# Optimization experiments

Measured on AMD Instinct MI355X. Metric: run time of the kernel, lower is better.

The kernel has to match this reference:

```python
import jax, jax.numpy as jnp
import numpy as np

D_MODEL = 1024
N_HEAD = 16
HEAD_SIZE = D_MODEL // N_HEAD


def setup_inputs() -> dict:
    key = jax.random.key(0)
    ks = jax.random.split(key, 7)
    B, T, E = 2, 2048, D_MODEL
    scale = 0.02
    return {
        "q": jax.random.normal(ks[0], (B, T, E), dtype=jnp.float32),
        "k": jax.random.normal(ks[1], (B, T, E), dtype=jnp.float32),
        "v": jax.random.normal(ks[2], (B, T, E), dtype=jnp.float32),
        "Wq": jax.random.normal(ks[3], (E, E), dtype=jnp.float32) * scale,
        "Wk": jax.random.normal(ks[4], (E, E), dtype=jnp.float32) * scale,
        "Wv": jax.random.normal(ks[5], (E, E), dtype=jnp.float32) * scale,
        "Wo": jax.random.normal(ks[6], (E, E), dtype=jnp.float32) * scale,
    }


def reference(q, k, v, Wq, Wk, Wv, Wo):
    B, T, E = q.shape
    # torch nn.Linear(bias=False): y = x @ W.T
    qh = (q @ Wq.T).reshape(B, T, N_HEAD, HEAD_SIZE).transpose(0, 2, 1, 3)  # [B,H,T,Dh]
    kh = (k @ Wk.T).reshape(B, T, N_HEAD, HEAD_SIZE).transpose(0, 2, 1, 3)
    vh = (v @ Wv.T).reshape(B, T, N_HEAD, HEAD_SIZE).transpose(0, 2, 1, 3)

    scale = 1.0 / jnp.sqrt(jnp.asarray(HEAD_SIZE, dtype=q.dtype))
    wei = jnp.einsum("bhqd,bhkd->bhqk", qh, kh) * scale  # [B,H,T,T]

    # causal mask (tril): positions j > i set to -inf
    causal = jnp.tril(jnp.ones((T, T), dtype=bool))
    wei = jnp.where(causal, wei, jnp.asarray(-jnp.inf, dtype=wei.dtype))

    attn = jax.nn.softmax(wei, axis=-1)
    out = jnp.einsum("bhqk,bhkd->bhqd", attn, vh)  # [B,H,T,Dh]
    out = out.transpose(0, 2, 1, 3).reshape(B, T, E)
    return out @ Wo.T  # dropout p=0.0 -> identity
```

## Files before the change

### kernel.cpp

```cpp
#include <hip/hip_runtime.h>
#include <hip/hip_bf16.h>
#include <cstddef>
#include <cstdint>

#define B_SZ   2
#define T_SEQ  2048
#define E_DIM  1024
#define N_HEAD 16
#define HEAD   64

typedef unsigned short u16;
typedef unsigned int u32;
using frag8 = __attribute__((ext_vector_type(8))) short;
using f32x4 = __attribute__((ext_vector_type(4))) float;

__device__ inline u16 f2bf(float x) {
    __hip_bfloat16 h = __float2bfloat16(x);
    return *reinterpret_cast<u16*>(&h);
}

__device__ inline void gl2lds16(const void* g, void* l) {
    auto gp = reinterpret_cast<const __attribute__((address_space(1))) unsigned int*>(
        reinterpret_cast<uintptr_t>(g));
    auto lp = reinterpret_cast<__attribute__((address_space(3))) unsigned int*>(
        reinterpret_cast<uintptr_t>(l));
    __builtin_amdgcn_global_load_lds(gp, lp, 16, 0, 0);
}

struct CastArgs {
    const float* src[7];
    u16* dst[7];
    int n[7];
    float scale[7];
};

__global__ __launch_bounds__(256) void cast_f32_bf16(CastArgs a) {
    const int t = blockIdx.y;
    const int i0 = (blockIdx.x * 256 + threadIdx.x) * 8;
    if (i0 >= a.n[t]) return;
    const float sc = a.scale[t];
    const float4 f0 = *(const float4*)(a.src[t] + i0);
    const float4 f1 = *(const float4*)(a.src[t] + i0 + 4);
    union { u16 s[8]; uint4 v; } r;
    r.s[0] = f2bf(f0.x * sc); r.s[1] = f2bf(f0.y * sc);
    r.s[2] = f2bf(f0.z * sc); r.s[3] = f2bf(f0.w * sc);
    r.s[4] = f2bf(f1.x * sc); r.s[5] = f2bf(f1.y * sc);
    r.s[6] = f2bf(f1.z * sc); r.s[7] = f2bf(f1.w * sc);
    *(uint4*)(a.dst[t] + i0) = r.v;
}

__device__ inline void gemm_core(const u16* __restrict__ X,
                                 const u16* __restrict__ W,
                                 void* __restrict__ Yv, int mode,
                                 int bm0, int bn0) {
    __shared__ u16 As[64 * 64];
    __shared__ u16 Bs[128 * 64];

    const int tid = threadIdx.x;
    const int w = tid >> 6;
    const int lane = tid & 63;
    const int ln = lane & 15;
    const int quad = lane >> 4;
    const int wm = (w & 1) * 32;
    const int wn = (w >> 1) * 64;

    const int l8 = lane >> 3;
    const int g = (lane & 7) ^ l8;

    const u16* Ag = X + (size_t)(bm0 + w * 16 + l8) * 1024 + g * 8;
    const u16* Bg = W + (size_t)(bn0 + w * 32 + l8) * 1024 + g * 8;
    const int al = __builtin_amdgcn_readfirstlane(w * 1024);
    const int bl = __builtin_amdgcn_readfirstlane(w * 2048);

    const f32x4 zf = {0.f, 0.f, 0.f, 0.f};
    f32x4 acc[2][4];
#pragma unroll
    for (int mi = 0; mi < 2; ++mi)
#pragma unroll
        for (int nj = 0; nj < 4; ++nj) acc[mi][nj] = zf;

    const int sw = ln & 7;

    for (int k0 = 0; k0 < 1024; k0 += 64) {
        gl2lds16(Ag + k0, As + al);
        gl2lds16(Ag + 8 * 1024 + k0, As + al + 512);
#pragma unroll
        for (int i = 0; i < 4; ++i)
            gl2lds16(Bg + i * 8 * 1024 + k0, Bs + bl + i * 512);
        __syncthreads();

        frag8 a[2][2], b[4][2];
#pragma unroll
        for (int kc = 0; kc < 2; ++kc) {
            const int slot = ((kc * 4 + quad) ^ sw) * 8;
#pragma unroll
            for (int mi = 0; mi < 2; ++mi)
                a[mi][kc] = *(const frag8*)(As + (wm + mi * 16 + ln) * 64 + slot);
#pragma unroll
            for (int nj = 0; nj < 4; ++nj)
                b[nj][kc] = *(const frag8*)(Bs + (wn + nj * 16 + ln) * 64 + slot);
        }
#pragma unroll
        for (int kc = 0; kc < 2; ++kc)
#pragma unroll
            for (int mi = 0; mi < 2; ++mi)
#pragma unroll
                for (int nj = 0; nj < 4; ++nj)
                    acc[mi][nj] = __builtin_amdgcn_mfma_f32_16x16x32_bf16(
                        a[mi][kc], b[nj][kc], acc[mi][nj], 0, 0, 0);
        __syncthreads();
    }

#pragma unroll
    for (int mi = 0; mi < 2; ++mi)
#pragma unroll
        for (int nj = 0; nj < 4; ++nj)
#pragma unroll
            for (int reg = 0; reg < 4; ++reg) {
                const int m = bm0 + wm + mi * 16 + quad * 4 + reg;
                const int n = bn0 + wn + nj * 16 + ln;
                if (mode == 1) {
                    ((float*)Yv)[(size_t)m * E_DIM + n] = acc[mi][nj][reg];
                } else {
                    const int b_ = m >> 11, t_ = m & (T_SEQ - 1);
                    const int h_ = n >> 6, d_ = n & (HEAD - 1);
                    const size_t idx = (mode == 0)
                        ? (((size_t)(b_ * N_HEAD + h_)) * T_SEQ + t_) * HEAD + d_
                        : (((size_t)(b_ * N_HEAD + h_)) * HEAD + d_) * T_SEQ + t_;
                    ((u16*)Yv)[idx] = f2bf(acc[mi][nj][reg]);
                }
            }
}

struct QkvArgs {
    const u16* X[3];
    const u16* W[3];
    u16* Y[3];
};

__global__ __launch_bounds__(256) void gemm_qkv(QkvArgs a) {
    const int z = blockIdx.z;
    gemm_core(a.X[z], a.W[z], a.Y[z], z == 2 ? 2 : 0,
              blockIdx.x * 64, blockIdx.y * 128);
}

__global__ __launch_bounds__(256) void gemm_out(const u16* __restrict__ X,
                                                const u16* __restrict__ W,
                                                float* __restrict__ Y) {
    gemm_core(X, W, Y, 1, blockIdx.x * 64, blockIdx.y * 128);
}

__global__ __launch_bounds__(256, 4) void attn_mfma(const u16* __restrict__ Qh,
                                                    const u16* __restrict__ Kh,
                                                    const u16* __restrict__ Vt_g,
                                                    u16* __restrict__ Aa) {
    __shared__ u16 Ks[2][64 * 64];
    __shared__ u16 Vs[2][64 * 64];

    const int tid = threadIdx.x;
    const int w = tid >> 6;
    const int lane = tid & 63;
    const int ln = lane & 15;
    const int quad = lane >> 4;

    const int i = blockIdx.x;
    const int half = i >> 8;
    const int r_ = i & 255;
    const int bh = r_ >> 3;
    const int j = r_ & 7;
    const int qt = half ? j : (15 - j);
    const int q0 = qt * 128;
    const int qw = q0 + w * 32;

    const size_t base = (size_t)bh * T_SEQ * HEAD;
    const u16* Qb = Qh + base;
    const u16* Kb = Kh + base;
    const u16* Vtb = Vt_g + base;

    const int l8 = lane >> 3;
    const int g = (lane & 7) ^ l8;
    const int kls = __builtin_amdgcn_readfirstlane(w * 16 * 64);
    const int vls = __builtin_amdgcn_readfirstlane(w * 16 * 64);

    frag8 qf[2][2];
#pragma unroll
    for (int qq = 0; qq < 2; ++qq)
#pragma unroll
        for (int kc = 0; kc < 2; ++kc)
            qf[qq][kc] = *(const frag8*)(Qb + (size_t)(qw + qq * 16 + ln) * HEAD +
                                         kc * 32 + quad * 8);

    const f32x4 zf = {0.f, 0.f, 0.f, 0.f};
    f32x4 o[4][2];
    float rsl[2] = {0.f, 0.f};
#pragma unroll
    for (int dt = 0; dt < 4; ++dt)
#pragma unroll
        for (int qq = 0; qq < 2; ++qq) o[dt][qq] = zf;

    const int ktiles = 2 * qt + 2;

    {
        const int k0 = 0;
#pragma unroll
        for (int it = 0; it < 2; ++it) {
            const int rb = w * 16 + it * 8;
            gl2lds16(Kb + (size_t)(k0 + rb + l8) * HEAD + g * 8,
                     &Ks[0][0] + kls + it * 512);
            gl2lds16(Vtb + (size_t)(rb + l8) * T_SEQ + k0 + g * 8,
                     &Vs[0][0] + vls + it * 512);
        }
    }

    const int sw = ln & 7;

    for (int kt = 0; kt < ktiles; ++kt) {
        const int k0 = kt * 64;
        const int buf = kt & 1;
        __syncthreads();

        if (kt + 1 < ktiles) {
            const int k1 = k0 + 64;
#pragma unroll
            for (int it = 0; it < 2; ++it) {
                const int rb = w * 16 + it * 8;
                gl2lds16(Kb + (size_t)(k1 + rb + l8) * HEAD + g * 8,
                         &Ks[buf ^ 1][0] + kls + it * 512);
                gl2lds16(Vtb + (size_t)(rb + l8) * T_SEQ + k1 + g * 8,
                         &Vs[buf ^ 1][0] + vls + it * 512);
            }
        }

        if (k0 <= qw + 31) {
            f32x4 st[4][2];
#pragma unroll
            for (int kk = 0; kk < 4; ++kk)
#pragma unroll
                for (int qq = 0; qq < 2; ++qq) st[kk][qq] = zf;
#pragma unroll
            for (int kc = 0; kc < 2; ++kc) {
                const int slot = ((kc * 4 + quad) ^ sw) * 8;
#pragma unroll
                for (int kk = 0; kk < 4; ++kk) {
                    const frag8 kf = *(const frag8*)(&Ks[buf][0] + (kk * 16 + ln) * 64 + slot);
#pragma unroll
                    for (int qq = 0; qq < 2; ++qq)
                        st[kk][qq] = __builtin_amdgcn_mfma_f32_16x16x32_bf16(
                            kf, qf[qq][kc], st[kk][qq], 0, 0, 0);
                }
            }

            const bool msk = (k0 + 63 > qw);
            u32 pk[4][2][2];
#pragma unroll
            for (int kk = 0; kk < 4; ++kk)
#pragma unroll
                for (int qq = 0; qq < 2; ++qq) {
                    float e[4];
#pragma unroll
                    for (int reg = 0; reg < 4; ++reg) {
                        const int key = k0 + kk * 16 + quad * 4 + reg;
                        const int qg = qw + qq * 16 + ln;
                        float ev = __expf(st[kk][qq][reg]);
                        if (msk) ev = (key <= qg) ? ev : 0.f;
                        e[reg] = ev;
                        rsl[qq] += ev;
                    }
                    pk[kk][qq][0] = ((u32)f2bf(e[1]) << 16) | f2bf(e[0]);
                    pk[kk][qq][1] = ((u32)f2bf(e[3]) << 16) | f2bf(e[2]);
                }

            const int hsel = quad >> 1;
            const int s_lo = ((quad & 1) * 2) * 16 + ln;
            const int s_hi = s_lo + 16;
#pragma unroll
            for (int kc = 0; kc < 2; ++kc) {
                union { frag8 f; u32 d[4]; } pb[2];
#pragma unroll
                for (int qq = 0; qq < 2; ++qq) {
                    const u32 a00 = __shfl(pk[kc * 2][qq][0], s_lo, 64);
                    const u32 a01 = __shfl(pk[kc * 2][qq][1], s_lo, 64);
                    const u32 a02 = __shfl(pk[kc * 2][qq][0], s_hi, 64);
                    const u32 a03 = __shfl(pk[kc * 2][qq][1], s_hi, 64);
                    const u32 a10 = __shfl(pk[kc * 2 + 1][qq][0], s_lo, 64);
                    const u32 a11 = __shfl(pk[kc * 2 + 1][qq][1], s_lo, 64);
                    const u32 a12 = __shfl(pk[kc * 2 + 1][qq][0], s_hi, 64);
                    const u32 a13 = __shfl(pk[kc * 2 + 1][qq][1], s_hi, 64);
                    pb[qq].d[0] = hsel ? a10 : a00;
                    pb[qq].d[1] = hsel ? a11 : a01;
                    pb[qq].d[2] = hsel ? a12 : a02;
                    pb[qq].d[3] = hsel ? a13 : a03;
                }
                const int slot = ((kc * 4 + quad) ^ sw) * 8;
#pragma unroll
                for (int dt = 0; dt < 4; ++dt) {
                    const frag8 vf = *(const frag8*)(&Vs[buf][0] + (dt * 16 + ln) * 64 + slot);
#pragma unroll
                    for (int qq = 0; qq < 2; ++qq)
                        o[dt][qq] = __builtin_amdgcn_mfma_f32_16x16x32_bf16(
                            vf, pb[qq].f, o[dt][qq], 0, 0, 0);
                }
            }
        }
    }

#pragma unroll
    for (int qq = 0; qq < 2; ++qq) {
        rsl[qq] += __shfl_xor(rsl[qq], 16, 64);
        rsl[qq] += __shfl_xor(rsl[qq], 32, 64);
    }
    const float inv0 = 1.f / rsl[0];
    const float inv1 = 1.f / rsl[1];
    const int b_ = bh >> 4, h_ = bh & (N_HEAD - 1);
#pragma unroll
    for (int qq = 0; qq < 2; ++qq) {
        const float inv = qq ? inv1 : inv0;
        const int qg = qw + qq * 16 + ln;
        u16* rowp = Aa + ((size_t)(b_ * T_SEQ + qg)) * E_DIM + h_ * HEAD;
#pragma unroll
        for (int dt = 0; dt < 4; ++dt)
#pragma unroll
            for (int rp = 0; rp < 2; ++rp) {
                const u32 v = ((u32)f2bf(o[dt][qq][2 * rp + 1] * inv) << 16) |
                              f2bf(o[dt][qq][2 * rp] * inv);
                *(u32*)(rowp + dt * 16 + quad * 4 + rp * 2) = v;
            }
    }
}

extern "C" void kernel_launch(void* const* d_in, const int* in_sizes, int n_in,
                              void* d_out, int out_size, void* d_ws, size_t ws_size,
                              hipStream_t stream) {
    const float* q  = (const float*)d_in[0];
    const float* k  = (const float*)d_in[1];
    const float* v  = (const float*)d_in[2];
    const float* Wq = (const float*)d_in[3];
    const float* Wk = (const float*)d_in[4];
    const float* Wv = (const float*)d_in[5];
    const float* Wo = (const float*)d_in[6];

    u16* ws = (u16*)d_ws;
    const size_t M4 = (size_t)4 * 1024 * 1024;
    const size_t M1 = (size_t)1024 * 1024;
    u16* qb  = ws;
    u16* kb  = ws + M4;
    u16* vb  = ws + 2 * M4;
    u16* Wqb = ws + 3 * M4;
    u16* Wkb = ws + 3 * M4 + M1;
    u16* Wvb = ws + 3 * M4 + 2 * M1;
    u16* Wob = ws + 3 * M4 + 3 * M1;
    u16* Qh  = ws + 4 * M4;
    u16* Kh  = ws + 5 * M4;
    u16* Vht = ws + 6 * M4;
    u16* Aa  = ws + 7 * M4;

    CastArgs ca;
    ca.src[0] = q;  ca.src[1] = k;  ca.src[2] = v;
    ca.src[3] = Wq; ca.src[4] = Wk; ca.src[5] = Wv; ca.src[6] = Wo;
    ca.dst[0] = qb;  ca.dst[1] = kb;  ca.dst[2] = vb;
    ca.dst[3] = Wqb; ca.dst[4] = Wkb; ca.dst[5] = Wvb; ca.dst[6] = Wob;
    ca.n[0] = ca.n[1] = ca.n[2] = (int)M4;
    ca.n[3] = ca.n[4] = ca.n[5] = ca.n[6] = (int)M1;
    ca.scale[0] = ca.scale[1] = ca.scale[2] = 1.f;
    ca.scale[3] = 0.125f;
    ca.scale[4] = ca.scale[5] = ca.scale[6] = 1.f;
    cast_f32_bf16<<<dim3(2048, 7), 256, 0, stream>>>(ca);

    QkvArgs ga;
    ga.X[0] = qb;  ga.X[1] = kb;  ga.X[2] = vb;
    ga.W[0] = Wqb; ga.W[1] = Wkb; ga.W[2] = Wvb;
    ga.Y[0] = Qh;  ga.Y[1] = Kh;  ga.Y[2] = Vht;
    gemm_qkv<<<dim3(64, 8, 3), 256, 0, stream>>>(ga);

    attn_mfma<<<dim3(512), 256, 0, stream>>>(Qh, Kh, Vht, Aa);

    gemm_out<<<dim3(64, 8), 256, 0, stream>>>(Aa, Wob, (float*)d_out);
}
```

Before: 220.3 us.

## Enlarge GEMM tiles to 128x128 and shrink attention query tiles to 64

```diff
diff --git a/kernel.cpp b/kernel.cpp
--- a/kernel.cpp
+++ b/kernel.cpp
@@ -53,7 +53,7 @@
                                  const u16* __restrict__ W,
                                  void* __restrict__ Yv, int mode,
                                  int bm0, int bn0) {
-    __shared__ u16 As[64 * 64];
+    __shared__ u16 As[128 * 64];
     __shared__ u16 Bs[128 * 64];
 
     const int tid = threadIdx.x;
@@ -61,49 +61,47 @@
     const int lane = tid & 63;
     const int ln = lane & 15;
     const int quad = lane >> 4;
-    const int wm = (w & 1) * 32;
+    const int wm = (w & 1) * 64;
     const int wn = (w >> 1) * 64;
 
     const int l8 = lane >> 3;
     const int g = (lane & 7) ^ l8;
 
-    const u16* Ag = X + (size_t)(bm0 + w * 16 + l8) * 1024 + g * 8;
+    const u16* Ag = X + (size_t)(bm0 + w * 32 + l8) * 1024 + g * 8;
     const u16* Bg = W + (size_t)(bn0 + w * 32 + l8) * 1024 + g * 8;
-    const int al = __builtin_amdgcn_readfirstlane(w * 1024);
-    const int bl = __builtin_amdgcn_readfirstlane(w * 2048);
+    const int sls = __builtin_amdgcn_readfirstlane(w * 32 * 64);
 
     const f32x4 zf = {0.f, 0.f, 0.f, 0.f};
-    f32x4 acc[2][4];
-#pragma unroll
-    for (int mi = 0; mi < 2; ++mi)
+    f32x4 acc[4][4];
+#pragma unroll
+    for (int mi = 0; mi < 4; ++mi)
 #pragma unroll
         for (int nj = 0; nj < 4; ++nj) acc[mi][nj] = zf;
 
     const int sw = ln & 7;
 
     for (int k0 = 0; k0 < 1024; k0 += 64) {
-        gl2lds16(Ag + k0, As + al);
-        gl2lds16(Ag + 8 * 1024 + k0, As + al + 512);
-#pragma unroll
-        for (int i = 0; i < 4; ++i)
-            gl2lds16(Bg + i * 8 * 1024 + k0, Bs + bl + i * 512);
+#pragma unroll
+        for (int it = 0; it < 4; ++it) {
+            gl2lds16(Ag + (size_t)it * 8 * 1024 + k0, As + sls + it * 512);
+            gl2lds16(Bg + (size_t)it * 8 * 1024 + k0, Bs + sls + it * 512);
+        }
         __syncthreads();
 
-        frag8 a[2][2], b[4][2];
+        frag8 a[4][2], b[4][2];
 #pragma unroll
         for (int kc = 0; kc < 2; ++kc) {
             const int slot = ((kc * 4 + quad) ^ sw) * 8;
 #pragma unroll
-            for (int mi = 0; mi < 2; ++mi)
-                a[mi][kc] = *(const frag8*)(As + (wm + mi * 16 + ln) * 64 + slot);
-#pragma unroll
-            for (int nj = 0; nj < 4; ++nj)
-                b[nj][kc] = *(const frag8*)(Bs + (wn + nj * 16 + ln) * 64 + slot);
+            for (int t = 0; t < 4; ++t) {
+                a[t][kc] = *(const frag8*)(As + (wm + t * 16 + ln) * 64 + slot);
+                b[t][kc] = *(const frag8*)(Bs + (wn + t * 16 + ln) * 64 + slot);
+            }
         }
 #pragma unroll
         for (int kc = 0; kc < 2; ++kc)
 #pragma unroll
-            for (int mi = 0; mi < 2; ++mi)
+            for (int mi = 0; mi < 4; ++mi)
 #pragma unroll
                 for (int nj = 0; nj < 4; ++nj)
                     acc[mi][nj] = __builtin_amdgcn_mfma_f32_16x16x32_bf16(
@@ -112,7 +110,7 @@
     }
 
 #pragma unroll
-    for (int mi = 0; mi < 2; ++mi)
+    for (int mi = 0; mi < 4; ++mi)
 #pragma unroll
         for (int nj = 0; nj < 4; ++nj)
 #pragma unroll
@@ -141,13 +139,13 @@
 __global__ __launch_bounds__(256) void gemm_qkv(QkvArgs a) {
     const int z = blockIdx.z;
     gemm_core(a.X[z], a.W[z], a.Y[z], z == 2 ? 2 : 0,
-              blockIdx.x * 64, blockIdx.y * 128);
+              blockIdx.x * 128, blockIdx.y * 128);
 }
 
 __global__ __launch_bounds__(256) void gemm_out(const u16* __restrict__ X,
                                                 const u16* __restrict__ W,
                                                 float* __restrict__ Y) {
-    gemm_core(X, W, Y, 1, blockIdx.x * 64, blockIdx.y * 128);
+    gemm_core(X, W, Y, 1, blockIdx.x * 128, blockIdx.y * 128);
 }
 
 __global__ __launch_bounds__(256, 4) void attn_mfma(const u16* __restrict__ Qh,
@@ -164,13 +162,13 @@
     const int quad = lane >> 4;
 
     const int i = blockIdx.x;
-    const int half = i >> 8;
-    const int r_ = i & 255;
-    const int bh = r_ >> 3;
-    const int j = r_ & 7;
-    const int qt = half ? j : (15 - j);
-    const int q0 = qt * 128;
-    const int qw = q0 + w * 32;
+    const int half = i >> 9;
+    const int r_ = i & 511;
+    const int bh = r_ >> 4;
+    const int j = r_ & 15;
+    const int qt = half ? j : (31 - j);
+    const int q0 = qt * 64;
+    const int qw = q0 + w * 16;
 
     const size_t base = (size_t)bh * T_SEQ * HEAD;
     const u16* Qb = Qh + base;
@@ -179,37 +177,26 @@
 
     const int l8 = lane >> 3;
     const int g = (lane & 7) ^ l8;
-    const int kls = __builtin_amdgcn_readfirstlane(w * 16 * 64);
-    const int vls = __builtin_amdgcn_readfirstlane(w * 16 * 64);
-
-    frag8 qf[2][2];
-#pragma unroll
-    for (int qq = 0; qq < 2; ++qq)
-#pragma unroll
-        for (int kc = 0; kc < 2; ++kc)
-            qf[qq][kc] = *(const frag8*)(Qb + (size_t)(qw + qq * 16 + ln) * HEAD +
-                                         kc * 32 + quad * 8);
+    const int sls = __builtin_amdgcn_readfirstlane(w * 16 * 64);
+
+    frag8 qf[2];
+#pragma unroll
+    for (int kc = 0; kc < 2; ++kc)
+        qf[kc] = *(const frag8*)(Qb + (size_t)(qw + ln) * HEAD + kc * 32 + quad * 8);
 
     const f32x4 zf = {0.f, 0.f, 0.f, 0.f};
-    f32x4 o[4][2];
-    float rsl[2] = {0.f, 0.f};
-#pragma unroll
-    for (int dt = 0; dt < 4; ++dt)
-#pragma unroll
-        for (int qq = 0; qq < 2; ++qq) o[dt][qq] = zf;
-
-    const int ktiles = 2 * qt + 2;
-
-    {
-        const int k0 = 0;
-#pragma unroll
-        for (int it = 0; it < 2; ++it) {
-            const int rb = w * 16 + it * 8;
-            gl2lds16(Kb + (size_t)(k0 + rb + l8) * HEAD + g * 8,
-                     &Ks[0][0] + kls + it * 512);
-            gl2lds16(Vtb + (size_t)(rb + l8) * T_SEQ + k0 + g * 8,
-                     &Vs[0][0] + vls + it * 512);
-        }
+    f32x4 o[4];
+    float rsl = 0.f;
+#pragma unroll
+    for (int dt = 0; dt < 4; ++dt) o[dt] = zf;
+
+    const int ktiles = qt + 1;
+
+#pragma unroll
+    for (int it = 0; it < 2; ++it) {
+        const int rb = w * 16 + it * 8;
+        gl2lds16(Kb + (size_t)(rb + l8) * HEAD + g * 8, &Ks[0][0] + sls + it * 512);
+        gl2lds16(Vtb + (size_t)(rb + l8) * T_SEQ + g * 8, &Vs[0][0] + sls + it * 512);
     }
 
     const int sw = ln & 7;
@@ -225,107 +212,86 @@
             for (int it = 0; it < 2; ++it) {
                 const int rb = w * 16 + it * 8;
                 gl2lds16(Kb + (size_t)(k1 + rb + l8) * HEAD + g * 8,
-                         &Ks[buf ^ 1][0] + kls + it * 512);
+                         &Ks[buf ^ 1][0] + sls + it * 512);
                 gl2lds16(Vtb + (size_t)(rb + l8) * T_SEQ + k1 + g * 8,
-                         &Vs[buf ^ 1][0] + vls + it * 512);
-            }
-        }
-
-        if (k0 <= qw + 31) {
-            f32x4 st[4][2];
-#pragma unroll
-            for (int kk = 0; kk < 4; ++kk)
-#pragma unroll
-                for (int qq = 0; qq < 2; ++qq) st[kk][qq] = zf;
-#pragma unroll
-            for (int kc = 0; kc < 2; ++kc) {
-                const int slot = ((kc * 4 + quad) ^ sw) * 8;
-#pragma unroll
-                for (int kk = 0; kk < 4; ++kk) {
-                    const frag8 kf = *(const frag8*)(&Ks[buf][0] + (kk * 16 + ln) * 64 + slot);
-#pragma unroll
-                    for (int qq = 0; qq < 2; ++qq)
-                        st[kk][qq] = __builtin_amdgcn_mfma_f32_16x16x32_bf16(
-                            kf, qf[qq][kc], st[kk][qq], 0, 0, 0);
-                }
-            }
-
-            const bool msk = (k0 + 63 > qw);
-            u32 pk[4][2][2];
-#pragma unroll
-            for (int kk = 0; kk < 4; ++kk)
-#pragma unroll
-                for (int qq = 0; qq < 2; ++qq) {
-                    float e[4];
-#pragma unroll
-                    for (int reg = 0; reg < 4; ++reg) {
-                        const int key = k0 + kk * 16 + quad * 4 + reg;
-                        const int qg = qw + qq * 16 + ln;
-                        float ev = __expf(st[kk][qq][reg]);
-                        if (msk) ev = (key <= qg) ? ev : 0.f;
-                        e[reg] = ev;
-                        rsl[qq] += ev;
-                    }
-                    pk[kk][qq][0] = ((u32)f2bf(e[1]) << 16) | f2bf(e[0]);
-                    pk[kk][qq][1] = ((u32)f2bf(e[3]) << 16) | f2bf(e[2]);
-                }
-
-            const int hsel = quad >> 1;
-            const int s_lo = ((quad & 1) * 2) * 16 + ln;
-            const int s_hi = s_lo + 16;
-#pragma unroll
-            for (int kc = 0; kc < 2; ++kc) {
-                union { frag8 f; u32 d[4]; } pb[2];
-#pragma unroll
-                for (int qq = 0; qq < 2; ++qq) {
-                    const u32 a00 = __shfl(pk[kc * 2][qq][0], s_lo, 64);
-                    const u32 a01 = __shfl(pk[kc * 2][qq][1], s_lo, 64);
-                    const u32 a02 = __shfl(pk[kc * 2][qq][0], s_hi, 64);
-                    const u32 a03 = __shfl(pk[kc * 2][qq][1], s_hi, 64);
-                    const u32 a10 = __shfl(pk[kc * 2 + 1][qq][0], s_lo, 64);
-                    const u32 a11 = __shfl(pk[kc * 2 + 1][qq][1], s_lo, 64);
-                    const u32 a12 = __shfl(pk[kc * 2 + 1][qq][0], s_hi, 64);
-                    const u32 a13 = __shfl(pk[kc * 2 + 1][qq][1], s_hi, 64);
-                    pb[qq].d[0] = hsel ? a10 : a00;
-                    pb[qq].d[1] = hsel ? a11 : a01;
-                    pb[qq].d[2] = hsel ? a12 : a02;
-                    pb[qq].d[3] = hsel ? a13 : a03;
-                }
-                const int slot = ((kc * 4 + quad) ^ sw) * 8;
-#pragma unroll
-                for (int dt = 0; dt < 4; ++dt) {
-                    const frag8 vf = *(const frag8*)(&Vs[buf][0] + (dt * 16 + ln) * 64 + slot);
-#pragma unroll
-                    for (int qq = 0; qq < 2; ++qq)
-                        o[dt][qq] = __builtin_amdgcn_mfma_f32_16x16x32_bf16(
-                            vf, pb[qq].f, o[dt][qq], 0, 0, 0);
-                }
+                         &Vs[buf ^ 1][0] + sls + it * 512);
+            }
+        }
+
+        f32x4 st[4];
+#pragma unroll
+        for (int kk = 0; kk < 4; ++kk) st[kk] = zf;
+#pragma unroll
+        for (int kc = 0; kc < 2; ++kc) {
+            const int slot = ((kc * 4 + quad) ^ sw) * 8;
+#pragma unroll
+            for (int kk = 0; kk < 4; ++kk) {
+                const frag8 kf = *(const frag8*)(&Ks[buf][0] + (kk * 16 + ln) * 64 + slot);
+                st[kk] = __builtin_amdgcn_mfma_f32_16x16x32_bf16(
+                    kf, qf[kc], st[kk], 0, 0, 0);
+            }
+        }
+
+        const bool diag = (kt == qt);
+        const int qg = qw + ln;
+        u32 pk[4][2];
+#pragma unroll
+        for (int kk = 0; kk < 4; ++kk) {
+            float e[4];
+#pragma unroll
+            for (int reg = 0; reg < 4; ++reg) {
+                const int key = k0 + kk * 16 + quad * 4 + reg;
+                float ev = __expf(st[kk][reg]);
+                if (diag) ev = (key <= qg) ? ev : 0.f;
+                e[reg] = ev;
+                rsl += ev;
+            }
+            pk[kk][0] = ((u32)f2bf(e[1]) << 16) | f2bf(e[0]);
+            pk[kk][1] = ((u32)f2bf(e[3]) << 16) | f2bf(e[2]);
+        }
+
+        const int hsel = quad >> 1;
+        const int s_lo = ((quad & 1) * 2) * 16 + ln;
+        const int s_hi = s_lo + 16;
+#pragma unroll
+        for (int kc = 0; kc < 2; ++kc) {
+            union { frag8 f; u32 d[4]; } pb;
+            const u32 a00 = __shfl(pk[kc * 2][0], s_lo, 64);
+            const u32 a01 = __shfl(pk[kc * 2][1], s_lo, 64);
+            const u32 a02 = __shfl(pk[kc * 2][0], s_hi, 64);
+            const u32 a03 = __shfl(pk[kc * 2][1], s_hi, 64);
+            const u32 a10 = __shfl(pk[kc * 2 + 1][0], s_lo, 64);
+            const u32 a11 = __shfl(pk[kc * 2 + 1][1], s_lo, 64);
+            const u32 a12 = __shfl(pk[kc * 2 + 1][0], s_hi, 64);
+            const u32 a13 = __shfl(pk[kc * 2 + 1][1], s_hi, 64);
+            pb.d[0] = hsel ? a10 : a00;
+            pb.d[1] = hsel ? a11 : a01;
+            pb.d[2] = hsel ? a12 : a02;
+            pb.d[3] = hsel ? a13 : a03;
+            const int slot = ((kc * 4 + quad) ^ sw) * 8;
+#pragma unroll
+            for (int dt = 0; dt < 4; ++dt) {
+                const frag8 vf = *(const frag8*)(&Vs[buf][0] + (dt * 16 + ln) * 64 + slot);
+                o[dt] = __builtin_amdgcn_mfma_f32_16x16x32_bf16(
+                    vf, pb.f, o[dt], 0, 0, 0);
             }
         }
     }
 
-#pragma unroll
-    for (int qq = 0; qq < 2; ++qq) {
-        rsl[qq] += __shfl_xor(rsl[qq], 16, 64);
-        rsl[qq] += __shfl_xor(rsl[qq], 32, 64);
-    }
-    const float inv0 = 1.f / rsl[0];
-    const float inv1 = 1.f / rsl[1];
+    rsl += __shfl_xor(rsl, 16, 64);
+    rsl += __shfl_xor(rsl, 32, 64);
+    const float inv = 1.f / rsl;
     const int b_ = bh >> 4, h_ = bh & (N_HEAD - 1);
-#pragma unroll
-    for (int qq = 0; qq < 2; ++qq) {
-        const float inv = qq ? inv1 : inv0;
-        const int qg = qw + qq * 16 + ln;
-        u16* rowp = Aa + ((size_t)(b_ * T_SEQ + qg)) * E_DIM + h_ * HEAD;
-#pragma unroll
-        for (int dt = 0; dt < 4; ++dt)
-#pragma unroll
-            for (int rp = 0; rp < 2; ++rp) {
-                const u32 v = ((u32)f2bf(o[dt][qq][2 * rp + 1] * inv) << 16) |
-                              f2bf(o[dt][qq][2 * rp] * inv);
-                *(u32*)(rowp + dt * 16 + quad * 4 + rp * 2) = v;
-            }
-    }
+    const int qg = qw + ln;
+    u16* rowp = Aa + ((size_t)(b_ * T_SEQ + qg)) * E_DIM + h_ * HEAD;
+#pragma unroll
+    for (int dt = 0; dt < 4; ++dt)
+#pragma unroll
+        for (int rp = 0; rp < 2; ++rp) {
+            const u32 v = ((u32)f2bf(o[dt][2 * rp + 1] * inv) << 16) |
+                          f2bf(o[dt][2 * rp] * inv);
+            *(u32*)(rowp + dt * 16 + quad * 4 + rp * 2) = v;
+        }
 }
 
 extern "C" void kernel_launch(void* const* d_in, const int* in_sizes, int n_in,
@@ -370,9 +336,9 @@
     ga.X[0] = qb;  ga.X[1] = kb;  ga.X[2] = vb;
     ga.W[0] = Wqb; ga.W[1] = Wkb; ga.W[2] = Wvb;
     ga.Y[0] = Qh;  ga.Y[1] = Kh;  ga.Y[2] = Vht;
-    gemm_qkv<<<dim3(64, 8, 3), 256, 0, stream>>>(ga);
-
-    attn_mfma<<<dim3(512), 256, 0, stream>>>(Qh, Kh, Vht, Aa);
-
-    gemm_out<<<dim3(64, 8), 256, 0, stream>>>(Aa, Wob, (float*)d_out);
-}
+    gemm_qkv<<<dim3(32, 8, 3), 256, 0, stream>>>(ga);
+
+    attn_mfma<<<dim3(1024), 256, 0, stream>>>(Qh, Kh, Vht, Aa);
+
+    gemm_out<<<dim3(32, 8), 256, 0, stream>>>(Aa, Wob, (float*)d_out);
+}
```

After: 235.6 us. 7.0% more time.

## Enlarge GEMM tiles to 128x128 and double-buffer LDS loads

Applied to the files above, without the earlier changes.

```diff
diff --git a/kernel.cpp b/kernel.cpp
--- a/kernel.cpp
+++ b/kernel.cpp
@@ -53,66 +53,75 @@
                                  const u16* __restrict__ W,
                                  void* __restrict__ Yv, int mode,
                                  int bm0, int bn0) {
-    __shared__ u16 As[64 * 64];
-    __shared__ u16 Bs[128 * 64];
+    __shared__ u16 As[2][128 * 64];
+    __shared__ u16 Bs[2][128 * 64];
 
     const int tid = threadIdx.x;
     const int w = tid >> 6;
     const int lane = tid & 63;
     const int ln = lane & 15;
     const int quad = lane >> 4;
-    const int wm = (w & 1) * 32;
+    const int wm = (w & 1) * 64;
     const int wn = (w >> 1) * 64;
 
     const int l8 = lane >> 3;
     const int g = (lane & 7) ^ l8;
 
-    const u16* Ag = X + (size_t)(bm0 + w * 16 + l8) * 1024 + g * 8;
+    const u16* Ag = X + (size_t)(bm0 + w * 32 + l8) * 1024 + g * 8;
     const u16* Bg = W + (size_t)(bn0 + w * 32 + l8) * 1024 + g * 8;
-    const int al = __builtin_amdgcn_readfirstlane(w * 1024);
-    const int bl = __builtin_amdgcn_readfirstlane(w * 2048);
+    const int sls = __builtin_amdgcn_readfirstlane(w * 32 * 64);
 
     const f32x4 zf = {0.f, 0.f, 0.f, 0.f};
-    f32x4 acc[2][4];
-#pragma unroll
-    for (int mi = 0; mi < 2; ++mi)
+    f32x4 acc[4][4];
+#pragma unroll
+    for (int mi = 0; mi < 4; ++mi)
 #pragma unroll
         for (int nj = 0; nj < 4; ++nj) acc[mi][nj] = zf;
 
     const int sw = ln & 7;
 
+#pragma unroll
+    for (int it = 0; it < 4; ++it) {
+        gl2lds16(Ag + (size_t)it * 8 * 1024, &As[0][0] + sls + it * 512);
+        gl2lds16(Bg + (size_t)it * 8 * 1024, &Bs[0][0] + sls + it * 512);
+    }
+
     for (int k0 = 0; k0 < 1024; k0 += 64) {
-        gl2lds16(Ag + k0, As + al);
-        gl2lds16(Ag + 8 * 1024 + k0, As + al + 512);
-#pragma unroll
-        for (int i = 0; i < 4; ++i)
-            gl2lds16(Bg + i * 8 * 1024 + k0, Bs + bl + i * 512);
+        const int buf = (k0 >> 6) & 1;
         __syncthreads();
 
-        frag8 a[2][2], b[4][2];
+        if (k0 + 64 < 1024) {
+#pragma unroll
+            for (int it = 0; it < 4; ++it) {
+                gl2lds16(Ag + (size_t)it * 8 * 1024 + k0 + 64,
+                         &As[buf ^ 1][0] + sls + it * 512);
+                gl2lds16(Bg + (size_t)it * 8 * 1024 + k0 + 64,
+                         &Bs[buf ^ 1][0] + sls + it * 512);
+            }
+        }
+
+        frag8 a[4][2], b[4][2];
 #pragma unroll
         for (int kc = 0; kc < 2; ++kc) {
             const int slot = ((kc * 4 + quad) ^ sw) * 8;
 #pragma unroll
-            for (int mi = 0; mi < 2; ++mi)
-                a[mi][kc] = *(const frag8*)(As + (wm + mi * 16 + ln) * 64 + slot);
-#pragma unroll
-            for (int nj = 0; nj < 4; ++nj)
-                b[nj][kc] = *(const frag8*)(Bs + (wn + nj * 16 + ln) * 64 + slot);
+            for (int t = 0; t < 4; ++t) {
+                a[t][kc] = *(const frag8*)(&As[buf][0] + (wm + t * 16 + ln) * 64 + slot);
+                b[t][kc] = *(const frag8*)(&Bs[buf][0] + (wn + t * 16 + ln) * 64 + slot);
+            }
         }
 #pragma unroll
         for (int kc = 0; kc < 2; ++kc)
 #pragma unroll
-            for (int mi = 0; mi < 2; ++mi)
+            for (int mi = 0; mi < 4; ++mi)
 #pragma unroll
                 for (int nj = 0; nj < 4; ++nj)
                     acc[mi][nj] = __builtin_amdgcn_mfma_f32_16x16x32_bf16(
                         a[mi][kc], b[nj][kc], acc[mi][nj], 0, 0, 0);
-        __syncthreads();
-    }
-
-#pragma unroll
-    for (int mi = 0; mi < 2; ++mi)
+    }
+
+#pragma unroll
+    for (int mi = 0; mi < 4; ++mi)
 #pragma unroll
         for (int nj = 0; nj < 4; ++nj)
 #pragma unroll
@@ -141,13 +150,13 @@
 __global__ __launch_bounds__(256) void gemm_qkv(QkvArgs a) {
     const int z = blockIdx.z;
     gemm_core(a.X[z], a.W[z], a.Y[z], z == 2 ? 2 : 0,
-              blockIdx.x * 64, blockIdx.y * 128);
+              blockIdx.x * 128, blockIdx.y * 128);
 }
 
 __global__ __launch_bounds__(256) void gemm_out(const u16* __restrict__ X,
                                                 const u16* __restrict__ W,
                                                 float* __restrict__ Y) {
-    gemm_core(X, W, Y, 1, blockIdx.x * 64, blockIdx.y * 128);
+    gemm_core(X, W, Y, 1, blockIdx.x * 128, blockIdx.y * 128);
 }
 
 __global__ __launch_bounds__(256, 4) void attn_mfma(const u16* __restrict__ Qh,
@@ -179,8 +188,7 @@
 
     const int l8 = lane >> 3;
     const int g = (lane & 7) ^ l8;
-    const int kls = __builtin_amdgcn_readfirstlane(w * 16 * 64);
-    const int vls = __builtin_amdgcn_readfirstlane(w * 16 * 64);
+    const int sls = __builtin_amdgcn_readfirstlane(w * 16 * 64);
 
     frag8 qf[2][2];
 #pragma unroll
@@ -200,16 +208,11 @@
 
     const int ktiles = 2 * qt + 2;
 
-    {
-        const int k0 = 0;
-#pragma unroll
-        for (int it = 0; it < 2; ++it) {
-            const int rb = w * 16 + it * 8;
-            gl2lds16(Kb + (size_t)(k0 + rb + l8) * HEAD + g * 8,
-                     &Ks[0][0] + kls + it * 512);
-            gl2lds16(Vtb + (size_t)(rb + l8) * T_SEQ + k0 + g * 8,
-                     &Vs[0][0] + vls + it * 512);
-        }
+#pragma unroll
+    for (int it = 0; it < 2; ++it) {
+        const int rb = w * 16 + it * 8;
+        gl2lds16(Kb + (size_t)(rb + l8) * HEAD + g * 8, &Ks[0][0] + sls + it * 512);
+        gl2lds16(Vtb + (size_t)(rb + l8) * T_SEQ + g * 8, &Vs[0][0] + sls + it * 512);
     }
 
     const int sw = ln & 7;
@@ -225,9 +228,9 @@
             for (int it = 0; it < 2; ++it) {
                 const int rb = w * 16 + it * 8;
                 gl2lds16(Kb + (size_t)(k1 + rb + l8) * HEAD + g * 8,
-                         &Ks[buf ^ 1][0] + kls + it * 512);
+                         &Ks[buf ^ 1][0] + sls + it * 512);
                 gl2lds16(Vtb + (size_t)(rb + l8) * T_SEQ + k1 + g * 8,
-                         &Vs[buf ^ 1][0] + vls + it * 512);
+                         &Vs[buf ^ 1][0] + sls + it * 512);
             }
         }
 
@@ -370,9 +373,9 @@
     ga.X[0] = qb;  ga.X[1] = kb;  ga.X[2] = vb;
     ga.W[0] = Wqb; ga.W[1] = Wkb; ga.W[2] = Wvb;
     ga.Y[0] = Qh;  ga.Y[1] = Kh;  ga.Y[2] = Vht;
-    gemm_qkv<<<dim3(64, 8, 3), 256, 0, stream>>>(ga);
+    gemm_qkv<<<dim3(32, 8, 3), 256, 0, stream>>>(ga);
 
     attn_mfma<<<dim3(512), 256, 0, stream>>>(Qh, Kh, Vht, Aa);
 
-    gemm_out<<<dim3(64, 8), 256, 0, stream>>>(Aa, Wob, (float*)d_out);
-}
+    gemm_out<<<dim3(32, 8), 256, 0, stream>>>(Aa, Wob, (float*)d_out);
+}
```

Measured after the change: 226.5 us. +2.8%, slower.

## Double-buffer GEMM LDS tiles and widen attention key tiles to 128

Applied to the files above, without the earlier changes.

```diff
diff --git a/kernel.cpp b/kernel.cpp
--- a/kernel.cpp
+++ b/kernel.cpp
@@ -53,8 +53,8 @@
                                  const u16* __restrict__ W,
                                  void* __restrict__ Yv, int mode,
                                  int bm0, int bn0) {
-    __shared__ u16 As[64 * 64];
-    __shared__ u16 Bs[128 * 64];
+    __shared__ u16 As[2][64 * 64];
+    __shared__ u16 Bs[2][128 * 64];
 
     const int tid = threadIdx.x;
     const int w = tid >> 6;
@@ -81,13 +81,24 @@
 
     const int sw = ln & 7;
 
+    gl2lds16(Ag, &As[0][0] + al);
+    gl2lds16(Ag + 8 * 1024, &As[0][0] + al + 512);
+#pragma unroll
+    for (int it = 0; it < 4; ++it)
+        gl2lds16(Bg + (size_t)it * 8 * 1024, &Bs[0][0] + bl + it * 512);
+
     for (int k0 = 0; k0 < 1024; k0 += 64) {
-        gl2lds16(Ag + k0, As + al);
-        gl2lds16(Ag + 8 * 1024 + k0, As + al + 512);
-#pragma unroll
-        for (int i = 0; i < 4; ++i)
-            gl2lds16(Bg + i * 8 * 1024 + k0, Bs + bl + i * 512);
+        const int buf = (k0 >> 6) & 1;
         __syncthreads();
+
+        if (k0 + 64 < 1024) {
+            gl2lds16(Ag + k0 + 64, &As[buf ^ 1][0] + al);
+            gl2lds16(Ag + 8 * 1024 + k0 + 64, &As[buf ^ 1][0] + al + 512);
+#pragma unroll
+            for (int it = 0; it < 4; ++it)
+                gl2lds16(Bg + (size_t)it * 8 * 1024 + k0 + 64,
+                         &Bs[buf ^ 1][0] + bl + it * 512);
+        }
 
         frag8 a[2][2], b[4][2];
 #pragma unroll
@@ -95,10 +106,10 @@
             const int slot = ((kc * 4 + quad) ^ sw) * 8;
 #pragma unroll
             for (int mi = 0; mi < 2; ++mi)
-                a[mi][kc] = *(const frag8*)(As + (wm + mi * 16 + ln) * 64 + slot);
+                a[mi][kc] = *(const frag8*)(&As[buf][0] + (wm + mi * 16 + ln) * 64 + slot);
 #pragma unroll
             for (int nj = 0; nj < 4; ++nj)
-                b[nj][kc] = *(const frag8*)(Bs + (wn + nj * 16 + ln) * 64 + slot);
+                b[nj][kc] = *(const frag8*)(&Bs[buf][0] + (wn + nj * 16 + ln) * 64 + slot);
         }
 #pragma unroll
         for (int kc = 0; kc < 2; ++kc)
@@ -108,7 +119,6 @@
                 for (int nj = 0; nj < 4; ++nj)
                     acc[mi][nj] = __builtin_amdgcn_mfma_f32_16x16x32_bf16(
                         a[mi][kc], b[nj][kc], acc[mi][nj], 0, 0, 0);
-        __syncthreads();
     }
 
 #pragma unroll
@@ -138,24 +148,24 @@
     u16* Y[3];
 };
 
-__global__ __launch_bounds__(256) void gemm_qkv(QkvArgs a) {
+__global__ __launch_bounds__(256, 3) void gemm_qkv(QkvArgs a) {
     const int z = blockIdx.z;
     gemm_core(a.X[z], a.W[z], a.Y[z], z == 2 ? 2 : 0,
               blockIdx.x * 64, blockIdx.y * 128);
 }
 
-__global__ __launch_bounds__(256) void gemm_out(const u16* __restrict__ X,
-                                                const u16* __restrict__ W,
-                                                float* __restrict__ Y) {
+__global__ __launch_bounds__(256, 3) void gemm_out(const u16* __restrict__ X,
+                                                   const u16* __restrict__ W,
+                                                   float* __restrict__ Y) {
     gemm_core(X, W, Y, 1, blockIdx.x * 64, blockIdx.y * 128);
 }
 
-__global__ __launch_bounds__(256, 4) void attn_mfma(const u16* __restrict__ Qh,
+__global__ __launch_bounds__(256, 2) void attn_mfma(const u16* __restrict__ Qh,
                                                     const u16* __restrict__ Kh,
                                                     const u16* __restrict__ Vt_g,
                                                     u16* __restrict__ Aa) {
-    __shared__ u16 Ks[2][64 * 64];
-    __shared__ u16 Vs[2][64 * 64];
+    __shared__ u16 Ks[2][128 * 64];
+    __shared__ u16 Vs[2][64 * 128];
 
     const int tid = threadIdx.x;
     const int w = tid >> 6;
@@ -178,9 +188,10 @@
     const u16* Vtb = Vt_g + base;
 
     const int l8 = lane >> 3;
-    const int g = (lane & 7) ^ l8;
-    const int kls = __builtin_amdgcn_readfirstlane(w * 16 * 64);
-    const int vls = __builtin_amdgcn_readfirstlane(w * 16 * 64);
+    const int gk = (lane & 7) ^ l8;
+    const int l16 = lane >> 4;
+    const int c16 = lane & 15;
+    const int sls = __builtin_amdgcn_readfirstlane(w * 2048);
 
     frag8 qf[2][2];
 #pragma unroll
@@ -198,108 +209,94 @@
 #pragma unroll
         for (int qq = 0; qq < 2; ++qq) o[dt][qq] = zf;
 
-    const int ktiles = 2 * qt + 2;
-
-    {
-        const int k0 = 0;
-#pragma unroll
-        for (int it = 0; it < 2; ++it) {
-            const int rb = w * 16 + it * 8;
-            gl2lds16(Kb + (size_t)(k0 + rb + l8) * HEAD + g * 8,
-                     &Ks[0][0] + kls + it * 512);
-            gl2lds16(Vtb + (size_t)(rb + l8) * T_SEQ + k0 + g * 8,
-                     &Vs[0][0] + vls + it * 512);
-        }
+    const int ktiles = qt + 1;
+
+#pragma unroll
+    for (int it = 0; it < 4; ++it) {
+        const int krow = w * 32 + it * 8 + l8;
+        gl2lds16(Kb + (size_t)krow * HEAD + gk * 8, &Ks[0][0] + sls + it * 512);
+        const int vrow = w * 16 + it * 4 + l16;
+        const int gv = c16 ^ (vrow & 7);
+        gl2lds16(Vtb + (size_t)vrow * T_SEQ + gv * 8, &Vs[0][0] + sls + it * 512);
     }
 
     const int sw = ln & 7;
+    const int hsel = quad >> 1;
+    const int s_lo = ((quad & 1) * 2) * 16 + ln;
+    const int s_hi = s_lo + 16;
 
     for (int kt = 0; kt < ktiles; ++kt) {
-        const int k0 = kt * 64;
+        const int k0 = kt << 7;
         const int buf = kt & 1;
         __syncthreads();
 
         if (kt + 1 < ktiles) {
-            const int k1 = k0 + 64;
-#pragma unroll
-            for (int it = 0; it < 2; ++it) {
-                const int rb = w * 16 + it * 8;
-                gl2lds16(Kb + (size_t)(k1 + rb + l8) * HEAD + g * 8,
-                         &Ks[buf ^ 1][0] + kls + it * 512);
-                gl2lds16(Vtb + (size_t)(rb + l8) * T_SEQ + k1 + g * 8,
-                         &Vs[buf ^ 1][0] + vls + it * 512);
-            }
-        }
-
-        if (k0 <= qw + 31) {
-            f32x4 st[4][2];
-#pragma unroll
-            for (int kk = 0; kk < 4; ++kk)
-#pragma unroll
-                for (int qq = 0; qq < 2; ++qq) st[kk][qq] = zf;
+            const int k1 = k0 + 128;
+#pragma unroll
+            for (int it = 0; it < 4; ++it) {
+                const int krow = w * 32 + it * 8 + l8;
+                gl2lds16(Kb + (size_t)(k1 + krow) * HEAD + gk * 8,
+                         &Ks[buf ^ 1][0] + sls + it * 512);
+                const int vrow = w * 16 + it * 4 + l16;
+                const int gv = c16 ^ (vrow & 7);
+                gl2lds16(Vtb + (size_t)vrow * T_SEQ + k1 + gv * 8,
+                         &Vs[buf ^ 1][0] + sls + it * 512);
+            }
+        }
+
+        const bool msk = (k0 + 127 > qw);
+        u32 pk[8][2][2];
+#pragma unroll
+        for (int kk = 0; kk < 8; ++kk) {
+            f32x4 st[2] = {zf, zf};
 #pragma unroll
             for (int kc = 0; kc < 2; ++kc) {
                 const int slot = ((kc * 4 + quad) ^ sw) * 8;
-#pragma unroll
-                for (int kk = 0; kk < 4; ++kk) {
-                    const frag8 kf = *(const frag8*)(&Ks[buf][0] + (kk * 16 + ln) * 64 + slot);
-#pragma unroll
-                    for (int qq = 0; qq < 2; ++qq)
-                        st[kk][qq] = __builtin_amdgcn_mfma_f32_16x16x32_bf16(
-                            kf, qf[qq][kc], st[kk][qq], 0, 0, 0);
+                const frag8 kf = *(const frag8*)(&Ks[buf][0] + (kk * 16 + ln) * 64 + slot);
+                st[0] = __builtin_amdgcn_mfma_f32_16x16x32_bf16(kf, qf[0][kc], st[0], 0, 0, 0);
+                st[1] = __builtin_amdgcn_mfma_f32_16x16x32_bf16(kf, qf[1][kc], st[1], 0, 0, 0);
+            }
+#pragma unroll
+            for (int qq = 0; qq < 2; ++qq) {
+                float e[4];
+#pragma unroll
+                for (int reg = 0; reg < 4; ++reg) {
+                    const int key = k0 + kk * 16 + quad * 4 + reg;
+                    const int qg = qw + qq * 16 + ln;
+                    float ev = __expf(st[qq][reg]);
+                    if (msk) ev = (key <= qg) ? ev : 0.f;
+                    e[reg] = ev;
+                    rsl[qq] += ev;
                 }
-            }
-
-            const bool msk = (k0 + 63 > qw);
-            u32 pk[4][2][2];
-#pragma unroll
-            for (int kk = 0; kk < 4; ++kk)
-#pragma unroll
-                for (int qq = 0; qq < 2; ++qq) {
-                    float e[4];
-#pragma unroll
-                    for (int reg = 0; reg < 4; ++reg) {
-                        const int key = k0 + kk * 16 + quad * 4 + reg;
-                        const int qg = qw + qq * 16 + ln;
-                        float ev = __expf(st[kk][qq][reg]);
-                        if (msk) ev = (key <= qg) ? ev : 0.f;
-                        e[reg] = ev;
-                        rsl[qq] += ev;
-                    }
-                    pk[kk][qq][0] = ((u32)f2bf(e[1]) << 16) | f2bf(e[0]);
-                    pk[kk][qq][1] = ((u32)f2bf(e[3]) << 16) | f2bf(e[2]);
-                }
-
-            const int hsel = quad >> 1;
-            const int s_lo = ((quad & 1) * 2) * 16 + ln;
-            const int s_hi = s_lo + 16;
-#pragma unroll
-            for (int kc = 0; kc < 2; ++kc) {
-                union { frag8 f; u32 d[4]; } pb[2];
-#pragma unroll
-                for (int qq = 0; qq < 2; ++qq) {
-                    const u32 a00 = __shfl(pk[kc * 2][qq][0], s_lo, 64);
-                    const u32 a01 = __shfl(pk[kc * 2][qq][1], s_lo, 64);
-                    const u32 a02 = __shfl(pk[kc * 2][qq][0], s_hi, 64);
-                    const u32 a03 = __shfl(pk[kc * 2][qq][1], s_hi, 64);
-                    const u32 a10 = __shfl(pk[kc * 2 + 1][qq][0], s_lo, 64);
-                    const u32 a11 = __shfl(pk[kc * 2 + 1][qq][1], s_lo, 64);
-                    const u32 a12 = __shfl(pk[kc * 2 + 1][qq][0], s_hi, 64);
-                    const u32 a13 = __shfl(pk[kc * 2 + 1][qq][1], s_hi, 64);
-                    pb[qq].d[0] = hsel ? a10 : a00;
-                    pb[qq].d[1] = hsel ? a11 : a01;
-                    pb[qq].d[2] = hsel ? a12 : a02;
-                    pb[qq].d[3] = hsel ? a13 : a03;
-                }
-                const int slot = ((kc * 4 + quad) ^ sw) * 8;
-#pragma unroll
-                for (int dt = 0; dt < 4; ++dt) {
-                    const frag8 vf = *(const frag8*)(&Vs[buf][0] + (dt * 16 + ln) * 64 + slot);
-#pragma unroll
-                    for (int qq = 0; qq < 2; ++qq)
-                        o[dt][qq] = __builtin_amdgcn_mfma_f32_16x16x32_bf16(
-                            vf, pb[qq].f, o[dt][qq], 0, 0, 0);
-                }
+                pk[kk][qq][0] = ((u32)f2bf(e[1]) << 16) | f2bf(e[0]);
+                pk[kk][qq][1] = ((u32)f2bf(e[3]) << 16) | f2bf(e[2]);
+            }
+        }
+
+#pragma unroll
+        for (int kc = 0; kc < 4; ++kc) {
+            union { frag8 f; u32 d[4]; } pb[2];
+#pragma unroll
+            for (int qq = 0; qq < 2; ++qq) {
+                const u32 a00 = __shfl(pk[kc * 2][qq][0], s_lo, 64);
+                const u32 a01 = __shfl(pk[kc * 2][qq][1], s_lo, 64);
+                const u32 a02 = __shfl(pk[kc * 2][qq][0], s_hi, 64);
+                const u32 a03 = __shfl(pk[kc * 2][qq][1], s_hi, 64);
+                const u32 a10 = __shfl(pk[kc * 2 + 1][qq][0], s_lo, 64);
+                const u32 a11 = __shfl(pk[kc * 2 + 1][qq][1], s_lo, 64);
+                const u32 a12 = __shfl(pk[kc * 2 + 1][qq][0], s_hi, 64);
+                const u32 a13 = __shfl(pk[kc * 2 + 1][qq][1], s_hi, 64);
+                pb[qq].d[0] = hsel ? a10 : a00;
+                pb[qq].d[1] = hsel ? a11 : a01;
+                pb[qq].d[2] = hsel ? a12 : a02;
+                pb[qq].d[3] = hsel ? a13 : a03;
+            }
+            const int slot = ((kc * 4 + quad) ^ sw) * 8;
+#pragma unroll
+            for (int dt = 0; dt < 4; ++dt) {
+                const frag8 vf = *(const frag8*)(&Vs[buf][0] + (dt * 16 + ln) * 128 + slot);
+                o[dt][0] = __builtin_amdgcn_mfma_f32_16x16x32_bf16(vf, pb[0].f, o[dt][0], 0, 0, 0);
+                o[dt][1] = __builtin_amdgcn_mfma_f32_16x16x32_bf16(vf, pb[1].f, o[dt][1], 0, 0, 0);
             }
         }
     }
```

Result: faster. 206.9 us (-6.0%).
